# Performance work log

Measured on AMD Instinct MI355X. Metric: run time of the kernel, lower is better.

Reference implementation:

```python
import jax, jax.numpy as jnp
import numpy as np

B, CIN, T, H, W = 4, 64, 8, 32, 32
COUT, AHID = 64, 16
HWF = H * W


def _conv2d(x, w, b):
    y = jax.lax.conv_general_dilated(x, w, (1, 1), [(1, 1), (1, 1)],
                                     dimension_numbers=("NCHW", "OIHW", "NCHW"))
    return y + b[None, :, None, None]


def _conv1x1(x, w, b):
    return jnp.einsum("bchw,oc->bohw", x, w) + b[None, :, None, None]


def setup_inputs():
    key = jax.random.key(0)
    ks = jax.random.split(key, 18)
    s = 0.05
    d = {}
    d["X"] = jax.random.normal(ks[0], (B, CIN, T, H, W), jnp.float32)
    d["conv_w"] = jax.random.normal(ks[1], (4 * COUT, CIN + COUT, 3, 3), jnp.float32) * s
    d["conv_b"] = jnp.zeros((4 * COUT,), jnp.float32)
    d["W_ci"] = jax.random.normal(ks[2], (COUT, H, W), jnp.float32) * s
    d["W_cf"] = jax.random.normal(ks[3], (COUT, H, W), jnp.float32) * s
    d["W_co"] = jax.random.normal(ks[4], (COUT, H, W), jnp.float32) * s
    d["q_w"] = jax.random.normal(ks[5], (AHID, COUT), jnp.float32) * s
    d["q_b"] = jnp.zeros((AHID,), jnp.float32)
    d["k_w"] = jax.random.normal(ks[6], (AHID, COUT), jnp.float32) * s
    d["k_b"] = jnp.zeros((AHID,), jnp.float32)
    d["k2_w"] = jax.random.normal(ks[7], (AHID, COUT), jnp.float32) * s
    d["k2_b"] = jnp.zeros((AHID,), jnp.float32)
    d["v_w"] = jax.random.normal(ks[8], (COUT, COUT), jnp.float32) * s
    d["v_b"] = jnp.zeros((COUT,), jnp.float32)
    d["v2_w"] = jax.random.normal(ks[9], (COUT, COUT), jnp.float32) * s
    d["v2_b"] = jnp.zeros((COUT,), jnp.float32)
    d["z_w"] = jax.random.normal(ks[10], (2 * COUT, 2 * COUT), jnp.float32) * s
    d["z_b"] = jnp.zeros((2 * COUT,), jnp.float32)
    d["m_w"] = jax.random.normal(ks[11], (3 * COUT, 3 * COUT), jnp.float32) * s
    d["m_b"] = jnp.zeros((3 * COUT,), jnp.float32)
    return d


def _forward(X, conv_w, conv_b, W_ci, W_cf, W_co, q_w, q_b, k_w, k_b, k2_w, k2_b,
             v_w, v_b, v2_w, v2_b, z_w, z_b, m_w, m_b):
    def step(carry, x_t):
        h, c, m = carry
        # ConvLSTM cell with peephole connections
        gates = _conv2d(jnp.concatenate([x_t, h], axis=1), conv_w, conv_b)
        i_c, f_c, g_c, o_c = jnp.split(gates, 4, axis=1)
        ig = jax.nn.sigmoid(i_c + W_ci * c)
        fg = jax.nn.sigmoid(f_c + W_cf * c)
        c_new = fg * c + ig * jnp.tanh(g_c)
        og = jax.nn.sigmoid(o_c + W_co * c_new)
        h_new = og * jnp.tanh(c_new)
        # Self-attention memory module (all projections are 1x1 convs)
        q = _conv1x1(h_new, q_w, q_b).reshape(B, AHID, HWF)
        kh = _conv1x1(h_new, k_w, k_b).reshape(B, AHID, HWF)
        vh = _conv1x1(h_new, v_w, v_b).reshape(B, COUT, HWF)
        km = _conv1x1(m, k2_w, k2_b).reshape(B, AHID, HWF)
        vm = _conv1x1(m, v2_w, v2_b).reshape(B, COUT, HWF)
        att_h = jax.nn.softmax(jnp.einsum("ban,bam->bnm", q, kh), axis=-1)  # (B,HW,HW)
        att_m = jax.nn.softmax(jnp.einsum("ban,bam->bnm", q, km), axis=-1)
        z_h = jnp.einsum("bnm,bcm->bcn", att_h, vh)  # (B,COUT,HW)
        z_m = jnp.einsum("bnm,bcm->bcn", att_m, vm)
        z = jnp.concatenate([z_h, z_m], axis=1).reshape(B, 2 * COUT, H, W)
        z = _conv1x1(z, z_w, z_b)
        comb = _conv1x1(jnp.concatenate([z, h_new], axis=1), m_w, m_b)
        mo, mg, mi = jnp.split(comb, 3, axis=1)
        gi = jax.nn.sigmoid(mi)
        m_new = (1.0 - gi) * m + gi * jnp.tanh(mg)
        h_out = jax.nn.sigmoid(mo) * m_new
        return (h_out, c_new, m_new), h_out

    zeros = jnp.zeros((B, COUT, H, W), X.dtype)
    Xs = jnp.moveaxis(X, 2, 0)  # (T, B, CIN, H, W)
    _, hs = jax.lax.scan(step, (zeros, zeros, zeros), Xs)
    return jnp.moveaxis(hs, 0, 2)  # (B, COUT, T, H, W)


def reference(X, conv_w, conv_b, W_ci, W_cf, W_co, q_w, q_b, k_w, k_b, k2_w, k2_b,
              v_w, v_b, v2_w, v2_b, z_w, z_b, m_w, m_b):
    return _forward(X, conv_w, conv_b, W_ci, W_cf, W_co, q_w, q_b, k_w, k_b,
                    k2_w, k2_b, v_w, v_b, v2_w, v2_b, z_w, z_b, m_w, m_b)
```

## Files before the change

kernel.cpp:

```cpp
#include <hip/hip_runtime.h>
#include <hip/hip_bf16.h>

typedef __hip_bfloat16 bf16;
typedef unsigned short ushort;
typedef __attribute__((ext_vector_type(8))) short short8v;
typedef __attribute__((ext_vector_type(4))) float float4v;

__device__ __forceinline__ float b2f(bf16 v){ return __bfloat162float(v); }
__device__ __forceinline__ float sigm(float x){ return 1.0f/(1.0f+__expf(-x)); }
__device__ __forceinline__ float tanhc(float x){
  x = fminf(15.0f, fmaxf(-15.0f, x));
  float e = __expf(2.0f*x);
  return (e-1.0f)/(e+1.0f);
}
__device__ __forceinline__ ushort f2bu(float f){
  bf16 h = __float2bfloat16(f); return *reinterpret_cast<ushort*>(&h);
}
__device__ __forceinline__ float bu2f(ushort u){
  return __uint_as_float(((unsigned)u)<<16);
}
__device__ __forceinline__ short8v ldfrag(const ushort* p){
  return *reinterpret_cast<const short8v*>(p);
}
__device__ __forceinline__ void glds16(const ushort* g, ushort* l){
  __builtin_amdgcn_global_load_lds(
    (const __attribute__((address_space(1))) unsigned int*)g,
    (__attribute__((address_space(3))) unsigned int*)l, 16, 0, 0);
}

#define WS_SMALL   0
#define WS_FLAG    262144
#define WS_ZROW    262160
#define WS_H       262208
#define WS_C       524352
#define WS_M       786496
#define WS_QB16    1310784
#define WS_KHB16   1376320
#define WS_KMB16   1441856
#define WS_VTH16   1507392
#define WS_VTM16   1638464
#define WS_MTH     1769536
#define WS_MTL     1900608
#define WS_HNTH    2031680
#define WS_HNTL    2162752
#define WS_ZW16H   2293824
#define WS_ZW16L   2302016
#define WS_MW16H   2310208
#define WS_MW16L   2328640
#define WS_WXAH    2347072
#define WS_WHAH    2420800
#define WS_WXAL    2494528
#define WS_WHAL    2568256
#define WS_XTHI    2641984
#define WS_XTLO    3690560
#define WS_HTHI    4739136
#define WS_HTLO    4870208
#define WS_PWH     5001280
#define WS_PWL     5006912
#define WS_GXG     5012544
#define WS_GXO     7109696
#define O_CB    0
#define O_WCI   256
#define O_WCF   65792
#define O_WCO   131328
#define O_QW    196864
#define O_QB    197888
#define O_KW    197904
#define O_KB    198928
#define O_K2W   198944
#define O_K2B   199968
#define O_VW    199984
#define O_VB    204080
#define O_V2W   204144
#define O_V2B   208240
#define O_ZW    208304
#define O_ZB    224688
#define O_MW    224816
#define O_MB    261680

__global__ void k_probe(const unsigned int* __restrict__ Xu, int* __restrict__ flag){
  __shared__ int cnt;
  if (threadIdx.x == 0) cnt = 0;
  __syncthreads();
  unsigned int u = Xu[threadIdx.x];
  float f = __uint_as_float((u & 0xffffu) << 16);
  int bad = (fabsf(f) <= 1e4f) ? 0 : 1;
  atomicAdd(&cnt, bad);
  __syncthreads();
  if (threadIdx.x == 0) *flag = (cnt > 16) ? 1 : 0;
}

struct P18 { const void* p[18]; };

__global__ __launch_bounds__(256) void k_wconv(P18 pk, const int* __restrict__ flagp,
                                               float* __restrict__ dst){
  const int ns[18]   = {256,65536,65536,65536,1024,16,1024,16,1024,16,
                        4096,64,4096,64,16384,128,36864,192};
  const int offs[18] = {O_CB,O_WCI,O_WCF,O_WCO,O_QW,O_QB,O_KW,O_KB,O_K2W,O_K2B,
                        O_VW,O_VB,O_V2W,O_V2B,O_ZW,O_ZB,O_MW,O_MB};
  int y = blockIdx.y;
  int n = ns[y];
  int flag = *flagp;
  const void* src = pk.p[y];
  for (int i = blockIdx.x*256 + threadIdx.x; i < n; i += gridDim.x*256){
    float v = flag ? ((const float*)src)[i] : b2f(((const bf16*)src)[i]);
    dst[offs[y] + i] = v;
  }
}

__global__ __launch_bounds__(256) void k_wtrans(float* __restrict__ ws){
  int i = blockIdx.x*256 + threadIdx.x;
  if (i < 16384){
    float f = ws[O_ZW + i];
    ushort h = f2bu(f);
    ((ushort*)(ws + WS_ZW16H))[i] = h;
    ((ushort*)(ws + WS_ZW16L))[i] = f2bu(f - bu2f(h));
  }
  if (i < 36864){
    float f = ws[O_MW + i];
    ushort h = f2bu(f);
    ((ushort*)(ws + WS_MW16H))[i] = h;
    ((ushort*)(ws + WS_MW16L))[i] = f2bu(f - bu2f(h));
  }
  if (i < 11264){
    int r = i >> 6, k = i & 63;
    float f;
    if (r < 16)       f = ws[O_QW  + r*64 + k];
    else if (r < 32)  f = ws[O_KW  + (r-16)*64 + k];
    else if (r < 48)  f = ws[O_K2W + (r-32)*64 + k];
    else if (r < 112) f = ws[O_VW  + (r-48)*64 + k];
    else              f = ws[O_V2W + (r-112)*64 + k];
    ushort h = f2bu(f);
    ((ushort*)(ws + WS_PWH))[i] = h;
    ((ushort*)(ws + WS_PWL))[i] = f2bu(f - bu2f(h));
  }
}

__global__ __launch_bounds__(256) void k_init(const void* __restrict__ conv_w,
                                              const int* __restrict__ flagp,
                                              float* __restrict__ ws){
  int i = blockIdx.x*256 + threadIdx.x;
  int flag = *flagp;
  if (i < 786432) ws[WS_H + i] = 0.0f;
  if (i < 32) ws[WS_ZROW + i] = 0.0f;
  if (i < 196608) ((unsigned*)(ws + WS_QB16))[i] = 0u;
  if (i < 294912){
    int ci = i & 127;
    int j = i >> 7;
    int mm = j & 255, p = j >> 8;
    int cc = mm >> 2, g = mm & 3;
    int si = ((g*64 + cc)*128 + ci)*9 + p;
    float f;
    ushort hi, lo = 0;
    if (flag){
      f = ((const float*)conv_w)[si];
      hi = f2bu(f);
      lo = f2bu(f - bu2f(hi));
    } else {
      hi = ((const ushort*)conv_w)[si];
    }
    if (ci < 64){
      int di = (j << 6) + ((((ci >> 3) ^ (mm & 7)) << 3) | (ci & 7));
      ((ushort*)(ws + WS_WXAH))[di] = hi;
      ((ushort*)(ws + WS_WXAL))[di] = lo;
    } else {
      int c2 = ci - 64;
      int di = (j << 6) + ((((c2 >> 3) ^ (mm & 7)) << 3) | (c2 & 7));
      ((ushort*)(ws + WS_WHAH))[di] = hi;
      ((ushort*)(ws + WS_WHAL))[di] = lo;
    }
  }
  if (i < 131072){
    ((unsigned*)(ws + WS_HTHI))[i] = 0u;
    ((unsigned*)(ws + WS_HTLO))[i] = 0u;
    ((unsigned*)(ws + WS_MTH))[i] = 0u;
    ((unsigned*)(ws + WS_MTL))[i] = 0u;
  }
}

__global__ __launch_bounds__(256) void k_xt(const void* __restrict__ Xraw,
                                            const int* __restrict__ flagp,
                                            float* __restrict__ ws){
  __shared__ ushort hi_s[64][66];
  __shared__ ushort lo_s[64][66];
  int pt = blockIdx.x, s = blockIdx.y;
  int b = s >> 3, t = s & 7;
  int flag = *flagp;
  int tid = threadIdx.x;
  for (int k = 0; k < 16; ++k){
    int idx = tid + k*256;
    int ci = idx >> 6, pxl = idx & 63;
    size_t si = ((size_t)(b*64 + ci)*8 + t)*1024 + pt*64 + pxl;
    if (flag){
      float f = ((const float*)Xraw)[si];
      ushort h = f2bu(f);
      hi_s[pxl][ci] = h;
      lo_s[pxl][ci] = f2bu(f - bu2f(h));
    } else {
      hi_s[pxl][ci] = ((const ushort*)Xraw)[si];
    }
  }
  __syncthreads();
  ushort* xh = (ushort*)(ws + WS_XTHI) + ((size_t)s*1024 + pt*64)*64;
  ushort* xl = (ushort*)(ws + WS_XTLO) + ((size_t)s*1024 + pt*64)*64;
  for (int k = 0; k < 16; ++k){
    int idx = tid + k*256;
    int pxl = idx >> 6, ci = idx & 63;
    xh[pxl*64 + ci] = hi_s[pxl][ci];
    if (flag) xl[pxl*64 + ci] = lo_s[pxl][ci];
  }
}

__global__ __launch_bounds__(512, 4) void k_convx(
  const int* __restrict__ flagp,
  const ushort* __restrict__ wxah, const ushort* __restrict__ wxal,
  const ushort* __restrict__ xt_hi, const ushort* __restrict__ xt_lo,
  float* __restrict__ gxg, ushort* __restrict__ gxo)
{
  __shared__ ushort xabuf[8192];
  __shared__ ushort xsm[54*136];
  int nt = blockIdx.x, mh = blockIdx.y, tb = blockIdx.z;
  int tid = threadIdx.x;
  int flag = *flagp;
  int ytile = nt >> 1, x0 = (nt & 1) * 16;
  const ushort* xb  = xt_hi + (size_t)tb*65536;
  const ushort* xlb = xt_lo + (size_t)tb*65536;
  int w = tid >> 6, lane = tid & 63, lr = lane & 15, lk = lane >> 4;
  const ushort* aw  = wxah + (size_t)(mh*128 + w*16)*64 + lane*8;
  const ushort* awl = wxal + (size_t)(mh*128 + w*16)*64 + lane*8;
  ushort* areg = xabuf + w*1024;

  const uint4 Z16 = make_uint4(0,0,0,0);
  for (int idx = tid; idx < 864; idx += 512){
    int slot = idx >> 4, c = idx & 15;
    int rr = slot / 18, xi = slot - rr*18;
    int gy = ytile - 1 + rr, gx2 = x0 - 1 + xi;
    bool valid = (gy >= 0) & (gy < 32) & (gx2 >= 0) & (gx2 < 32);
    int px = gy*32 + gx2;
    uint4 v = Z16;
    if (valid){
      if (c < 8)       v = *reinterpret_cast<const uint4*>(xb  + (size_t)px*64 + c*8);
      else if (flag)   v = *reinterpret_cast<const uint4*>(xlb + (size_t)px*64 + (c-8)*8);
    }
    *reinterpret_cast<uint4*>(&xsm[slot*136 + c*8]) = v;
  }
  __syncthreads();

  int px = nt*16 + lr;
  int sw = lr & 7;
  const int cx0 = ((lk ^ sw) << 3);
  const int cx1 = (((4+lk) ^ sw) << 3);
  float4v acc = {0.f,0.f,0.f,0.f};

  #pragma unroll 1
  for (int p = 0; p < 9; ++p){
    glds16(aw + (size_t)p*16384,       areg);
    glds16(aw + (size_t)p*16384 + 512, areg + 512);
    asm volatile("s_waitcnt vmcnt(0)" ::: "memory");
    __builtin_amdgcn_sched_barrier(0);
    short8v A0 = ldfrag(areg + lr*64 + cx0);
    short8v A1 = ldfrag(areg + lr*64 + cx1);
    int pinl = (p/3)*18 + lr + (p%3);
    const ushort* bl = &xsm[pinl*136 + lk*8];
    short8v BX0 = ldfrag(bl), BX1 = ldfrag(bl+32);
    acc = __builtin_amdgcn_mfma_f32_16x16x32_bf16(A0, BX0, acc, 0,0,0);
    acc = __builtin_amdgcn_mfma_f32_16x16x32_bf16(A1, BX1, acc, 0,0,0);
    if (flag){
      short8v BXl0 = ldfrag(bl+64), BXl1 = ldfrag(bl+96);
      acc = __builtin_amdgcn_mfma_f32_16x16x32_bf16(A0, BXl0, acc, 0,0,0);
      acc = __builtin_amdgcn_mfma_f32_16x16x32_bf16(A1, BXl1, acc, 0,0,0);
      asm volatile("s_waitcnt lgkmcnt(0)" ::: "memory");
      __builtin_amdgcn_sched_barrier(0);
      glds16(awl + (size_t)p*16384,       areg);
      glds16(awl + (size_t)p*16384 + 512, areg + 512);
      asm volatile("s_waitcnt vmcnt(0)" ::: "memory");
      __builtin_amdgcn_sched_barrier(0);
      short8v Al0 = ldfrag(areg + lr*64 + cx0);
      short8v Al1 = ldfrag(areg + lr*64 + cx1);
      acc = __builtin_amdgcn_mfma_f32_16x16x32_bf16(Al0, BX0, acc, 0,0,0);
      acc = __builtin_amdgcn_mfma_f32_16x16x32_bf16(Al1, BX1, acc, 0,0,0);
      asm volatile("s_waitcnt lgkmcnt(0)" ::: "memory");
      __builtin_amdgcn_sched_barrier(0);
    } else {
      asm volatile("s_waitcnt lgkmcnt(0)" ::: "memory");
      __builtin_amdgcn_sched_barrier(0);
    }
  }

  {
    int cc = mh*32 + w*4 + lk;
    gxg[((size_t)tb*64 + cc)*1024 + px] = acc[2];
    ushort* go = gxo + ((size_t)tb*192 + cc*3)*1024 + px;
    go[0]    = f2bu(acc[0]);
    go[1024] = f2bu(acc[1]);
    go[2048] = f2bu(acc[3]);
  }
}

__global__ __launch_bounds__(1024, 4) void k_convp(
  const int* __restrict__ flagp,
  const ushort* __restrict__ whah, const ushort* __restrict__ whal,
  const ushort* __restrict__ ht_hi, const ushort* __restrict__ ht_lo,
  const float* __restrict__ gxg, const ushort* __restrict__ gxo,
  const float* __restrict__ smalls, float* __restrict__ cst,
  const ushort* __restrict__ pwh, const ushort* __restrict__ pwl,
  const ushort* __restrict__ mth, const ushort* __restrict__ mtl,
  ushort* __restrict__ hnth, ushort* __restrict__ hntl,
  ushort* __restrict__ qb16, ushort* __restrict__ khb16, ushort* __restrict__ kmb16,
  ushort* __restrict__ vth16, ushort* __restrict__ vtm16, int t)
{
  __shared__ ushort albuf[16384];
  __shared__ ushort bsm[54*136];
  __shared__ ushort hbh[16*72];
  __shared__ ushort hbl[16*72];
  int nt = blockIdx.x, b = blockIdx.y;
  int tid = threadIdx.x;
  int flag = *flagp;
  int ytile = nt >> 1, x0 = (nt & 1) * 16;

  const ushort* hb  = ht_hi + (size_t)b*65536;
  const ushort* hlb = ht_lo + (size_t)b*65536;

  int w = tid >> 6, lane = tid & 63, lr = lane & 15, lk = lane >> 4;
  const ushort* aw  = whah + (size_t)(w*16)*64 + lane*8;
  const ushort* awl = whal + (size_t)(w*16)*64 + lane*8;
  ushort* areg = albuf + w*1024;

  if (!flag){
    glds16(aw, areg);
    glds16(aw + 512, areg + 512);
  }

  int px = nt*16 + lr;
  int cc = w*4 + lk;
  int tb = b*8 + t;
  const ushort* go = gxo + ((size_t)tb*192 + cc*3)*1024 + px;
  float a0 = bu2f(go[0]);
  float a1 = bu2f(go[1024]);
  float a3 = bu2f(go[2048]);
  float a2 = gxg[((size_t)tb*64 + cc)*1024 + px];

  const uint4 Z16 = make_uint4(0,0,0,0);
  if (tid < 864){
    int slot = tid >> 4, c = tid & 15;
    int rr = slot / 18, xi = slot - rr*18;
    int gy = ytile - 1 + rr, gx2 = x0 - 1 + xi;
    bool valid = (gy >= 0) & (gy < 32) & (gx2 >= 0) & (gx2 < 32);
    int hpx = gy*32 + gx2;
    uint4 v = Z16;
    if (valid){
      if (c < 8) v = *reinterpret_cast<const uint4*>(hb  + (size_t)hpx*64 + c*8);
      else       v = *reinterpret_cast<const uint4*>(hlb + (size_t)hpx*64 + (c-8)*8);
    }
    *reinterpret_cast<uint4*>(&bsm[slot*136 + c*8]) = v;
  }
  __syncthreads();

  const int sw = lr & 7;
  const int c2n = ((lk ^ sw) << 3);
  const int c3n = (((4+lk) ^ sw) << 3);

  float4v acc = {a0, a1, a2, a3};

  if (!flag){
    #pragma unroll
    for (int p = 0; p < 9; ++p){
      if (p > 0){
        asm volatile("s_waitcnt vmcnt(0)" ::: "memory");
        __builtin_amdgcn_sched_barrier(0);
      }
      short8v A2 = ldfrag(areg + lr*64 + c2n);
      short8v A3 = ldfrag(areg + lr*64 + c3n);
      if (p < 8){
        asm volatile("s_waitcnt lgkmcnt(0)" ::: "memory");
        __builtin_amdgcn_sched_barrier(0);
        glds16(aw + (size_t)(p+1)*16384,       areg);
        glds16(aw + (size_t)(p+1)*16384 + 512, areg + 512);
        __builtin_amdgcn_sched_barrier(0);
      }
      int pinl = (p/3)*18 + lr + (p%3);
      const ushort* bl = &bsm[pinl*136 + lk*8];
      short8v BH0 = ldfrag(bl),    BH1 = ldfrag(bl+32);
      short8v BL0 = ldfrag(bl+64), BL1 = ldfrag(bl+96);
      acc = __builtin_amdgcn_mfma_f32_16x16x32_bf16(A2, BH0, acc, 0,0,0);
      acc = __builtin_amdgcn_mfma_f32_16x16x32_bf16(A3, BH1, acc, 0,0,0);
      acc = __builtin_amdgcn_mfma_f32_16x16x32_bf16(A2, BL0, acc, 0,0,0);
      acc = __builtin_amdgcn_mfma_f32_16x16x32_bf16(A3, BL1, acc, 0,0,0);
    }
  } else {
    #pragma unroll 1
    for (int p = 0; p < 9; ++p){
      glds16(aw + (size_t)p*16384,       areg);
      glds16(aw + (size_t)p*16384 + 512, areg + 512);
      asm volatile("s_waitcnt vmcnt(0)" ::: "memory");
      __builtin_amdgcn_sched_barrier(0);
      short8v A2 = ldfrag(areg + lr*64 + c2n);
      short8v A3 = ldfrag(areg + lr*64 + c3n);
      asm volatile("s_waitcnt lgkmcnt(0)" ::: "memory");
      __builtin_amdgcn_sched_barrier(0);
      glds16(awl + (size_t)p*16384,       areg);
      glds16(awl + (size_t)p*16384 + 512, areg + 512);
      asm volatile("s_waitcnt vmcnt(0)" ::: "memory");
      __builtin_amdgcn_sched_barrier(0);
      short8v Al2 = ldfrag(areg + lr*64 + c2n);
      short8v Al3 = ldfrag(areg + lr*64 + c3n);
      asm volatile("s_waitcnt lgkmcnt(0)" ::: "memory");
      __builtin_amdgcn_sched_barrier(0);
      int pinl = (p/3)*18 + lr + (p%3);
      const ushort* bl = &bsm[pinl*136 + lk*8];
      short8v BH0 = ldfrag(bl),    BH1 = ldfrag(bl+32);
      short8v BL0 = ldfrag(bl+64), BL1 = ldfrag(bl+96);
      acc = __builtin_amdgcn_mfma_f32_16x16x32_bf16(A2, BH0, acc, 0,0,0);
      acc = __builtin_amdgcn_mfma_f32_16x16x32_bf16(A3, BH1, acc, 0,0,0);
      acc = __builtin_amdgcn_mfma_f32_16x16x32_bf16(A2, BL0, acc, 0,0,0);
      acc = __builtin_amdgcn_mfma_f32_16x16x32_bf16(A3, BL1, acc, 0,0,0);
      acc = __builtin_amdgcn_mfma_f32_16x16x32_bf16(Al2, BH0, acc, 0,0,0);
      acc = __builtin_amdgcn_mfma_f32_16x16x32_bf16(Al3, BH1, acc, 0,0,0);
    }
  }

  {
    int wi = cc*1024 + px;
    size_t sidx = ((size_t)(b*64 + cc))*1024 + px;
    float cprev = cst[sidx];
    float ic = acc[0] + smalls[O_CB + cc];
    float fc = acc[1] + smalls[O_CB + 64 + cc];
    float gc = acc[2] + smalls[O_CB + 128 + cc];
    float oc = acc[3] + smalls[O_CB + 192 + cc];
    float ig = sigm(ic + smalls[O_WCI + wi]*cprev);
    float fg = sigm(fc + smalls[O_WCF + wi]*cprev);
    float cnew = fg*cprev + ig*tanhc(gc);
    float og = sigm(oc + smalls[O_WCO + wi]*cnew);
    cst[sidx] = cnew;
    float hv = og*tanhc(cnew);
    size_t tix = ((size_t)b*1024 + px)*64 + cc;
    ushort hh = f2bu(hv);
    ushort hl2 = f2bu(hv - bu2f(hh));
    hnth[tix] = hh;
    hntl[tix] = hl2;
    hbh[lr*72 + cc] = hh;
    hbl[lr*72 + cc] = hl2;
  }
  __syncthreads();

  if (w < 11){
    int tt = w;
    const float4v Z4 = {0.f,0.f,0.f,0.f};
    bool srcm = (tt == 2) || (tt >= 7);
    short8v b0, b1, bl0, bl1;
    if (srcm){
      size_t bb = ((size_t)b*1024 + nt*16 + lr)*64 + lk*8;
      b0  = ldfrag(mth + bb);  b1  = ldfrag(mth + bb + 32);
      bl0 = ldfrag(mtl + bb);  bl1 = ldfrag(mtl + bb + 32);
    } else {
      b0  = ldfrag(&hbh[lr*72 + lk*8]);  b1  = ldfrag(&hbh[lr*72 + 32 + lk*8]);
      bl0 = ldfrag(&hbl[lr*72 + lk*8]);  bl1 = ldfrag(&hbl[lr*72 + 32 + lk*8]);
    }
    const ushort* ar = pwh + (size_t)(tt*16 + lr)*64 + lk*8;
    short8v pa0 = ldfrag(ar), pa1 = ldfrag(ar + 32);
    float4v d = Z4;
    d = __builtin_amdgcn_mfma_f32_16x16x32_bf16(pa0, b0,  d, 0,0,0);
    d = __builtin_amdgcn_mfma_f32_16x16x32_bf16(pa1, b1,  d, 0,0,0);
    d = __builtin_amdgcn_mfma_f32_16x16x32_bf16(pa0, bl0, d, 0,0,0);
    d = __builtin_amdgcn_mfma_f32_16x16x32_bf16(pa1, bl1, d, 0,0,0);
    if (flag){
      const ushort* arl = pwl + (size_t)(tt*16 + lr)*64 + lk*8;
      short8v pal0 = ldfrag(arl), pal1 = ldfrag(arl + 32);
      d = __builtin_amdgcn_mfma_f32_16x16x32_bf16(pal0, b0, d, 0,0,0);
      d = __builtin_amdgcn_mfma_f32_16x16x32_bf16(pal1, b1, d, 0,0,0);
    }
    int n = nt*16 + lr;
    int boff = (tt==0) ? O_QB : (tt==1) ? O_KB : (tt==2) ? O_K2B
             : (tt<7) ? (O_VB + (tt-3)*16) : (O_V2B + (tt-7)*16);
    if (tt < 3){
      ushort* base = (tt==0) ? qb16 : (tt==1) ? khb16 : kmb16;
      ushort u[4];
      #pragma unroll
      for (int q = 0; q < 4; ++q)
        u[q] = f2bu(d[q] + smalls[boff + lk*4 + q]);
      *reinterpret_cast<uint2*>(&base[((size_t)b*1024 + n)*32 + lk*4]) =
        make_uint2((unsigned)u[0] | ((unsigned)u[1]<<16),
                   (unsigned)u[2] | ((unsigned)u[3]<<16));
    } else {
      ushort* base = (tt<7) ? vth16 : vtm16;
      int cc0 = ((tt<7) ? (tt-3) : (tt-7))*16 + lk*4;
      #pragma unroll
      for (int q = 0; q < 4; ++q)
        base[((size_t)b*64 + cc0 + q)*1024 + n] = f2bu(d[q] + smalls[boff + lk*4 + q]);
    }
  }
}

__global__ __launch_bounds__(512) void k_fattz(
  const ushort* __restrict__ qb16, const ushort* __restrict__ khb16,
  const ushort* __restrict__ kmb16, const ushort* __restrict__ vth16,
  const ushort* __restrict__ vtm16,
  const ushort* __restrict__ hnth, const ushort* __restrict__ hntl,
  const float* __restrict__ smalls,
  const ushort* __restrict__ zw16h, const ushort* __restrict__ zw16l,
  const ushort* __restrict__ mw16h, const ushort* __restrict__ mw16l,
  const int* __restrict__ flagp,
  float* __restrict__ mst, ushort* __restrict__ mth, ushort* __restrict__ mtl,
  ushort* __restrict__ hth, ushort* __restrict__ htl,
  void* __restrict__ outraw, int t)
{
  __shared__ __align__(16) unsigned char poolA[34816];
  __shared__ __align__(16) ushort ztbh[16*136];
  __shared__ __align__(16) ushort ztbl[16*136];
  __shared__ float cb[192*17];
  __shared__ float ml[64*17];
  __shared__ float rs_s[2][4][16];

  ushort* es   = (ushort*)poolA;
  ushort* zbh  = (ushort*)poolA;
  ushort* zbl  = (ushort*)(poolA + 8704);
  float*  ho_s = (float*)poolA;
  float*  mn_s = (float*)(poolA + 4352);

  int nt = blockIdx.x, b = blockIdx.y;
  int n0 = nt*16;
  int tid = threadIdx.x;
  int w = tid >> 6, lane = tid & 63, lr = lane & 15, lk = lane >> 4;
  int br = w >> 2, wq = w & 3;
  int flag = *flagp;
  const float4v Z4 = {0.f,0.f,0.f,0.f};

  const ushort* kb = (br ? kmb16 : khb16) + (size_t)b*32768;
  const ushort* vt = (br ? vtm16 : vth16) + (size_t)b*65536;
  const ushort* qp = qb16 + (size_t)b*32768;

  for (int idx = tid; idx < 1024; idx += 512){
    int ch = idx >> 4, pp = idx & 15;
    ml[ch*17+pp] = mst[((size_t)b*64 + ch)*1024 + n0 + pp];
  }

  short8v qf = ldfrag(qp + (size_t)(n0 + lr)*32 + lk*8);

  float4v acc[2];
  acc[0]=Z4; acc[1]=Z4;
  float rsum = 0.f;

  #pragma unroll 1
  for (int mc = 0; mc < 4; ++mc){
    ushort* esb = es + (br*2 + (mc & 1))*4352;
    int mbase = mc*256 + wq*64;
    #pragma unroll
    for (int tau = 0; tau < 4; ++tau){
      short8v af = ldfrag(kb + (size_t)(mbase + tau*16 + lr)*32 + lk*8);
      float4v d = __builtin_amdgcn_mfma_f32_16x16x32_bf16(af, qf, Z4, 0,0,0);
      ushort u0 = f2bu(__expf(fminf(d[0], 60.f)));
      ushort u1 = f2bu(__expf(fminf(d[1], 60.f)));
      ushort u2 = f2bu(__expf(fminf(d[2], 60.f)));
      ushort u3 = f2bu(__expf(fminf(d[3], 60.f)));
      rsum += (bu2f(u0) + bu2f(u1)) + (bu2f(u2) + bu2f(u3));
      unsigned lo = (unsigned)u0 | ((unsigned)u1 << 16);
      unsigned hi = (unsigned)u2 | ((unsigned)u3 << 16);
      *reinterpret_cast<uint2*>(&esb[lr*272 + wq*64 + tau*16 + lk*4]) = make_uint2(lo, hi);
    }
    __syncthreads();
    #pragma unroll
    for (int ks = 0; ks < 8; ++ks){
      short8v av = ldfrag(vt + (size_t)(wq*16 + lr)*1024 + mc*256 + ks*32 + lk*8);
      short8v bv = ldfrag(&esb[lr*272 + ks*32 + lk*8]);
      acc[ks & 1] = __builtin_amdgcn_mfma_f32_16x16x32_bf16(av, bv, acc[ks & 1], 0,0,0);
    }
  }

  {
    float r = rsum;
    r += __shfl_xor(r, 16);
    r += __shfl_xor(r, 32);
    if (lane < 16) rs_s[br][wq][lr] = r;
  }
  __syncthreads();
  {
    float rinv = 1.0f / (rs_s[br][0][lr] + rs_s[br][1][lr] + rs_s[br][2][lr] + rs_s[br][3][lr]);
    int ch0 = br*64 + wq*16 + lk*4;
    ushort uh[4], ul[4];
    #pragma unroll
    for (int r = 0; r < 4; ++r){
      float z = (acc[0][r] + acc[1][r])*rinv;
      uh[r] = f2bu(z);
      ul[r] = f2bu(z - bu2f(uh[r]));
    }
    *reinterpret_cast<uint2*>(&zbh[lr*136 + ch0]) =
      make_uint2((unsigned)uh[0] | ((unsigned)uh[1]<<16), (unsigned)uh[2] | ((unsigned)uh[3]<<16));
    *reinterpret_cast<uint2*>(&zbl[lr*136 + ch0]) =
      make_uint2((unsigned)ul[0] | ((unsigned)ul[1]<<16), (unsigned)ul[2] | ((unsigned)ul[3]<<16));
  }
  __syncthreads();

  {
    float4v zacc = Z4;
    if (!flag){
      #pragma unroll
      for (int kf = 0; kf < 4; ++kf){
        short8v a  = ldfrag(zw16h + (size_t)(w*16 + lr)*128 + kf*32 + lk*8);
        short8v bh = ldfrag(&zbh[lr*136 + kf*32 + lk*8]);
        short8v bl = ldfrag(&zbl[lr*136 + kf*32 + lk*8]);
        zacc = __builtin_amdgcn_mfma_f32_16x16x32_bf16(a, bh, zacc, 0,0,0);
        zacc = __builtin_amdgcn_mfma_f32_16x16x32_bf16(a, bl, zacc, 0,0,0);
      }
    } else {
      #pragma unroll
      for (int kf = 0; kf < 4; ++kf){
        short8v a  = ldfrag(zw16h + (size_t)(w*16 + lr)*128 + kf*32 + lk*8);
        short8v al = ldfrag(zw16l + (size_t)(w*16 + lr)*128 + kf*32 + lk*8);
        short8v bh = ldfrag(&zbh[lr*136 + kf*32 + lk*8]);
        short8v bl = ldfrag(&zbl[lr*136 + kf*32 + lk*8]);
        zacc = __builtin_amdgcn_mfma_f32_16x16x32_bf16(a,  bh, zacc, 0,0,0);
        zacc = __builtin_amdgcn_mfma_f32_16x16x32_bf16(a,  bl, zacc, 0,0,0);
        zacc = __builtin_amdgcn_mfma_f32_16x16x32_bf16(al, bh, zacc, 0,0,0);
      }
    }
    int r0 = w*16 + lk*4;
    ushort th[4], tl[4];
    #pragma unroll
    for (int q = 0; q < 4; ++q){
      float ztv = zacc[q] + smalls[O_ZB + r0 + q];
      th[q] = f2bu(ztv);
      tl[q] = f2bu(ztv - bu2f(th[q]));
    }
    *reinterpret_cast<uint2*>(&ztbh[lr*136 + r0]) =
      make_uint2((unsigned)th[0] | ((unsigned)th[1]<<16), (unsigned)th[2] | ((unsigned)th[3]<<16));
    *reinterpret_cast<uint2*>(&ztbl[lr*136 + r0]) =
      make_uint2((unsigned)tl[0] | ((unsigned)tl[1]<<16), (unsigned)tl[2] | ((unsigned)tl[3]<<16));
  }
  __syncthreads();

  const ushort* hrow  = hnth + ((size_t)b*1024 + n0 + lr)*64;
  const ushort* hrowl = hntl + ((size_t)b*1024 + n0 + lr)*64;
  #pragma unroll
  for (int mi = 0; mi < 2; ++mi){
    if (mi == 1 && w >= 4) break;
    int mf = (mi == 0) ? w : (w + 8);
    float4v cacc = Z4;
    const ushort* arow  = mw16h + (size_t)(mf*16 + lr)*192;
    const ushort* arowl = mw16l + (size_t)(mf*16 + lr)*192;
    if (!flag){
      #pragma unroll
      for (int kf = 0; kf < 4; ++kf){
        short8v a  = ldfrag(arow + kf*32 + lk*8);
        short8v bh = ldfrag(&ztbh[lr*136 + kf*32 + lk*8]);
        short8v bl = ldfrag(&ztbl[lr*136 + kf*32 + lk*8]);
        cacc = __builtin_amdgcn_mfma_f32_16x16x32_bf16(a, bh, cacc, 0,0,0);
        cacc = __builtin_amdgcn_mfma_f32_16x16x32_bf16(a, bl, cacc, 0,0,0);
      }
      #pragma unroll
      for (int kf = 0; kf < 2; ++kf){
        short8v a  = ldfrag(arow + 128 + kf*32 + lk*8);
        short8v bh = ldfrag(hrow + kf*32 + lk*8);
        short8v bl = ldfrag(hrowl + kf*32 + lk*8);
        cacc = __builtin_amdgcn_mfma_f32_16x16x32_bf16(a, bh, cacc, 0,0,0);
        cacc = __builtin_amdgcn_mfma_f32_16x16x32_bf16(a, bl, cacc, 0,0,0);
      }
    } else {
      #pragma unroll
      for (int kf = 0; kf < 4; ++kf){
        short8v a  = ldfrag(arow + kf*32 + lk*8);
        short8v al = ldfrag(arowl + kf*32 + lk*8);
        short8v bh = ldfrag(&ztbh[lr*136 + kf*32 + lk*8]);
        short8v bl = ldfrag(&ztbl[lr*136 + kf*32 + lk*8]);
        cacc = __builtin_amdgcn_mfma_f32_16x16x32_bf16(a,  bh, cacc, 0,0,0);
        cacc = __builtin_amdgcn_mfma_f32_16x16x32_bf16(a,  bl, cacc, 0,0,0);
        cacc = __builtin_amdgcn_mfma_f32_16x16x32_bf16(al, bh, cacc, 0,0,0);
      }
      #pragma unroll
      for (int kf = 0; kf < 2; ++kf){
        short8v a  = ldfrag(arow + 128 + kf*32 + lk*8);
        short8v al = ldfrag(arowl + 128 + kf*32 + lk*8);
        short8v bh = ldfrag(hrow + kf*32 + lk*8);
        short8v bl = ldfrag(hrowl + kf*32 + lk*8);
        cacc = __builtin_amdgcn_mfma_f32_16x16x32_bf16(a,  bh, cacc, 0,0,0);
        cacc = __builtin_amdgcn_mfma_f32_16x16x32_bf16(a,  bl, cacc, 0,0,0);
        cacc = __builtin_amdgcn_mfma_f32_16x16x32_bf16(al, bh, cacc, 0,0,0);
      }
    }
    int r0 = mf*16 + lk*4;
    #pragma unroll
    for (int q = 0; q < 4; ++q)
      cb[(r0+q)*17 + lr] = cacc[q] + smalls[O_MB + r0 + q];
  }
  __syncthreads();

  {
    int px = tid >> 5, lr2 = tid & 31;
    #pragma unroll
    for (int j = 0; j < 2; ++j){
      int ch = lr2 + 32*j;
      float mo = cb[ch*17 + px];
      float mg = cb[(64+ch)*17 + px];
      float mi = cb[(128+ch)*17 + px];
      float mold = ml[ch*17 + px];
      float gi = sigm(mi);
      float mnew = (1.0f-gi)*mold + gi*tanhc(mg);
      float ho = sigm(mo)*mnew;
      ho_s[ch*17+px] = ho;
      mn_s[ch*17+px] = mnew;
    }
  }
  __syncthreads();
  for (int idx = tid; idx < 1024; idx += 512){
    int ch = idx >> 4, pp = idx & 15;
    int n = n0 + pp;
    size_t gidx = ((size_t)b*64 + ch)*1024 + n;
    float mn = mn_s[ch*17+pp];
    mst[gidx] = mn;
    float ho = ho_s[ch*17+pp];
    size_t tix = ((size_t)b*1024 + n)*64 + ch;
    ushort hb_ = f2bu(ho);
    hth[tix] = hb_;
    htl[tix] = f2bu(ho - bu2f(hb_));
    ushort mh_ = f2bu(mn);
    mth[tix] = mh_;
    mtl[tix] = f2bu(mn - bu2f(mh_));
    size_t oidx = ((size_t)(b*64+ch)*8 + t)*1024 + n;
    if (flag) ((float*)outraw)[oidx] = ho;
    else      ((bf16*)outraw)[oidx] = __float2bfloat16(ho);
  }
}

extern "C" void kernel_launch(void* const* d_in, const int* in_sizes, int n_in,
                              void* d_out, int out_size, void* d_ws, size_t ws_size,
                              hipStream_t stream)
{
  float* ws = (float*)d_ws;
  int* flag = (int*)(ws + WS_FLAG);
  float* c    = ws + WS_C;
  float* m    = ws + WS_M;
  float* gxg  = ws + WS_GXG;
  ushort* gxo   = (ushort*)(ws + WS_GXO);
  ushort* qb16  = (ushort*)(ws + WS_QB16);
  ushort* khb16 = (ushort*)(ws + WS_KHB16);
  ushort* kmb16 = (ushort*)(ws + WS_KMB16);
  ushort* vth16 = (ushort*)(ws + WS_VTH16);
  ushort* vtm16 = (ushort*)(ws + WS_VTM16);
  ushort* mth   = (ushort*)(ws + WS_MTH);
  ushort* mtl   = (ushort*)(ws + WS_MTL);
  ushort* hnth  = (ushort*)(ws + WS_HNTH);
  ushort* hntl  = (ushort*)(ws + WS_HNTL);
  ushort* zw16h = (ushort*)(ws + WS_ZW16H);
  ushort* zw16l = (ushort*)(ws + WS_ZW16L);
  ushort* mw16h = (ushort*)(ws + WS_MW16H);
  ushort* mw16l = (ushort*)(ws + WS_MW16L);
  ushort* wxah  = (ushort*)(ws + WS_WXAH);
  ushort* wxal  = (ushort*)(ws + WS_WXAL);
  ushort* whah  = (ushort*)(ws + WS_WHAH);
  ushort* whal  = (ushort*)(ws + WS_WHAL);
  ushort* xt_hi = (ushort*)(ws + WS_XTHI);
  ushort* xt_lo = (ushort*)(ws + WS_XTLO);
  ushort* ht_hi = (ushort*)(ws + WS_HTHI);
  ushort* ht_lo = (ushort*)(ws + WS_HTLO);
  ushort* pwh   = (ushort*)(ws + WS_PWH);
  ushort* pwl   = (ushort*)(ws + WS_PWL);

  k_probe<<<1, 256, 0, stream>>>((const unsigned int*)d_in[0], flag);
  P18 pk;
  for (int i = 0; i < 18; ++i) pk.p[i] = d_in[2 + i];
  k_wconv<<<dim3(64,18), 256, 0, stream>>>(pk, flag, ws);
  k_init<<<3072, 256, 0, stream>>>(d_in[1], flag, ws);
  k_xt<<<dim3(16,32), 256, 0, stream>>>(d_in[0], flag, ws);
  k_wtrans<<<144, 256, 0, stream>>>(ws);
  k_convx<<<dim3(64,2,32), 512, 0, stream>>>(flag, wxah, wxal, xt_hi, xt_lo, gxg, gxo);

  for (int t = 0; t < 8; ++t){
    k_convp<<<dim3(64,4), 1024, 0, stream>>>(flag, whah, whal, ht_hi, ht_lo,
                                             gxg, gxo, ws, c, pwh, pwl, mth, mtl,
                                             hnth, hntl, qb16, khb16, kmb16,
                                             vth16, vtm16, t);
    k_fattz<<<dim3(64,4), 512, 0, stream>>>(qb16, khb16, kmb16, vth16, vtm16,
                                            hnth, hntl, ws, zw16h, zw16l, mw16h, mw16l,
                                            flag, m, mth, mtl, ht_hi, ht_lo, d_out, t);
  }
  (void)in_sizes; (void)n_in; (void)out_size; (void)ws_size;
}
```

Baseline: 404.4 us.

## Double-buffer weight tiles in x-convolution and split flag path into phases

```diff
diff --git a/kernel.cpp b/kernel.cpp
--- a/kernel.cpp
+++ b/kernel.cpp
@@ -217,8 +217,8 @@
   const ushort* __restrict__ xt_hi, const ushort* __restrict__ xt_lo,
   float* __restrict__ gxg, ushort* __restrict__ gxo)
 {
-  __shared__ ushort xabuf[8192];
-  __shared__ ushort xsm[54*136];
+  __shared__ ushort xabuf[16384];
+  __shared__ ushort xsm[54*72];
   int nt = blockIdx.x, mh = blockIdx.y, tb = blockIdx.z;
   int tid = threadIdx.x;
   int flag = *flagp;
@@ -228,21 +228,24 @@
   int w = tid >> 6, lane = tid & 63, lr = lane & 15, lk = lane >> 4;
   const ushort* aw  = wxah + (size_t)(mh*128 + w*16)*64 + lane*8;
   const ushort* awl = wxal + (size_t)(mh*128 + w*16)*64 + lane*8;
-  ushort* areg = xabuf + w*1024;
+  ushort* buf0 = xabuf + w*1024;
+  ushort* buf1 = xabuf + 8192 + w*1024;
 
   const uint4 Z16 = make_uint4(0,0,0,0);
-  for (int idx = tid; idx < 864; idx += 512){
-    int slot = idx >> 4, c = idx & 15;
+
+  if (!flag){
+    glds16(aw, buf0);
+    glds16(aw + 512, buf0 + 512);
+  }
+
+  for (int idx = tid; idx < 432; idx += 512){
+    int slot = idx >> 3, c = idx & 7;
     int rr = slot / 18, xi = slot - rr*18;
     int gy = ytile - 1 + rr, gx2 = x0 - 1 + xi;
     bool valid = (gy >= 0) & (gy < 32) & (gx2 >= 0) & (gx2 < 32);
     int px = gy*32 + gx2;
-    uint4 v = Z16;
-    if (valid){
-      if (c < 8)       v = *reinterpret_cast<const uint4*>(xb  + (size_t)px*64 + c*8);
-      else if (flag)   v = *reinterpret_cast<const uint4*>(xlb + (size_t)px*64 + (c-8)*8);
-    }
-    *reinterpret_cast<uint4*>(&xsm[slot*136 + c*8]) = v;
+    uint4 v = valid ? *reinterpret_cast<const uint4*>(xb + (size_t)px*64 + c*8) : Z16;
+    *reinterpret_cast<uint4*>(&xsm[slot*72 + c*8]) = v;
   }
   __syncthreads();
 
@@ -252,36 +255,74 @@
   const int cx1 = (((4+lk) ^ sw) << 3);
   float4v acc = {0.f,0.f,0.f,0.f};
 
-  #pragma unroll 1
-  for (int p = 0; p < 9; ++p){
-    glds16(aw + (size_t)p*16384,       areg);
-    glds16(aw + (size_t)p*16384 + 512, areg + 512);
-    asm volatile("s_waitcnt vmcnt(0)" ::: "memory");
-    __builtin_amdgcn_sched_barrier(0);
-    short8v A0 = ldfrag(areg + lr*64 + cx0);
-    short8v A1 = ldfrag(areg + lr*64 + cx1);
-    int pinl = (p/3)*18 + lr + (p%3);
-    const ushort* bl = &xsm[pinl*136 + lk*8];
-    short8v BX0 = ldfrag(bl), BX1 = ldfrag(bl+32);
-    acc = __builtin_amdgcn_mfma_f32_16x16x32_bf16(A0, BX0, acc, 0,0,0);
-    acc = __builtin_amdgcn_mfma_f32_16x16x32_bf16(A1, BX1, acc, 0,0,0);
-    if (flag){
-      short8v BXl0 = ldfrag(bl+64), BXl1 = ldfrag(bl+96);
-      acc = __builtin_amdgcn_mfma_f32_16x16x32_bf16(A0, BXl0, acc, 0,0,0);
-      acc = __builtin_amdgcn_mfma_f32_16x16x32_bf16(A1, BXl1, acc, 0,0,0);
-      asm volatile("s_waitcnt lgkmcnt(0)" ::: "memory");
+  if (!flag){
+    #pragma unroll
+    for (int p = 0; p < 9; ++p){
+      if (p < 8){
+        ushort* dst = (p & 1) ? buf0 : buf1;
+        glds16(aw + (size_t)(p+1)*16384,       dst);
+        glds16(aw + (size_t)(p+1)*16384 + 512, dst + 512);
+        asm volatile("s_waitcnt vmcnt(2)" ::: "memory");
+      } else {
+        asm volatile("s_waitcnt vmcnt(0)" ::: "memory");
+      }
       __builtin_amdgcn_sched_barrier(0);
-      glds16(awl + (size_t)p*16384,       areg);
-      glds16(awl + (size_t)p*16384 + 512, areg + 512);
+      const ushort* ab = (p & 1) ? buf1 : buf0;
+      short8v A0 = ldfrag(ab + lr*64 + cx0);
+      short8v A1 = ldfrag(ab + lr*64 + cx1);
+      int pinl = (p/3)*18 + lr + (p%3);
+      const ushort* bl = &xsm[pinl*72 + lk*8];
+      short8v BX0 = ldfrag(bl), BX1 = ldfrag(bl+32);
+      acc = __builtin_amdgcn_mfma_f32_16x16x32_bf16(A0, BX0, acc, 0,0,0);
+      acc = __builtin_amdgcn_mfma_f32_16x16x32_bf16(A1, BX1, acc, 0,0,0);
+    }
+  } else {
+    #pragma unroll 1
+    for (int p = 0; p < 9; ++p){
+      glds16(aw  + (size_t)p*16384,       buf0);
+      glds16(aw  + (size_t)p*16384 + 512, buf0 + 512);
+      glds16(awl + (size_t)p*16384,       buf1);
+      glds16(awl + (size_t)p*16384 + 512, buf1 + 512);
       asm volatile("s_waitcnt vmcnt(0)" ::: "memory");
       __builtin_amdgcn_sched_barrier(0);
-      short8v Al0 = ldfrag(areg + lr*64 + cx0);
-      short8v Al1 = ldfrag(areg + lr*64 + cx1);
+      short8v A0  = ldfrag(buf0 + lr*64 + cx0);
+      short8v A1  = ldfrag(buf0 + lr*64 + cx1);
+      short8v Al0 = ldfrag(buf1 + lr*64 + cx0);
+      short8v Al1 = ldfrag(buf1 + lr*64 + cx1);
+      int pinl = (p/3)*18 + lr + (p%3);
+      const ushort* bl = &xsm[pinl*72 + lk*8];
+      short8v BX0 = ldfrag(bl), BX1 = ldfrag(bl+32);
+      acc = __builtin_amdgcn_mfma_f32_16x16x32_bf16(A0,  BX0, acc, 0,0,0);
+      acc = __builtin_amdgcn_mfma_f32_16x16x32_bf16(A1,  BX1, acc, 0,0,0);
       acc = __builtin_amdgcn_mfma_f32_16x16x32_bf16(Al0, BX0, acc, 0,0,0);
       acc = __builtin_amdgcn_mfma_f32_16x16x32_bf16(Al1, BX1, acc, 0,0,0);
       asm volatile("s_waitcnt lgkmcnt(0)" ::: "memory");
       __builtin_amdgcn_sched_barrier(0);
-    } else {
+    }
+    __syncthreads();
+    for (int idx = tid; idx < 432; idx += 512){
+      int slot = idx >> 3, c = idx & 7;
+      int rr = slot / 18, xi = slot - rr*18;
+      int gy = ytile - 1 + rr, gx2 = x0 - 1 + xi;
+      bool valid = (gy >= 0) & (gy < 32) & (gx2 >= 0) & (gx2 < 32);
+      int hp = gy*32 + gx2;
+      uint4 v = valid ? *reinterpret_cast<const uint4*>(xlb + (size_t)hp*64 + c*8) : Z16;
+      *reinterpret_cast<uint4*>(&xsm[slot*72 + c*8]) = v;
+    }
+    __syncthreads();
+    #pragma unroll 1
+    for (int p = 0; p < 9; ++p){
+      glds16(aw + (size_t)p*16384,       buf0);
+      glds16(aw + (size_t)p*16384 + 512, buf0 + 512);
+      asm volatile("s_waitcnt vmcnt(0)" ::: "memory");
+      __builtin_amdgcn_sched_barrier(0);
+      short8v A0 = ldfrag(buf0 + lr*64 + cx0);
+      short8v A1 = ldfrag(buf0 + lr*64 + cx1);
+      int pinl = (p/3)*18 + lr + (p%3);
+      const ushort* bl = &xsm[pinl*72 + lk*8];
+      short8v BXl0 = ldfrag(bl), BXl1 = ldfrag(bl+32);
+      acc = __builtin_amdgcn_mfma_f32_16x16x32_bf16(A0, BXl0, acc, 0,0,0);
+      acc = __builtin_amdgcn_mfma_f32_16x16x32_bf16(A1, BXl1, acc, 0,0,0);
       asm volatile("s_waitcnt lgkmcnt(0)" ::: "memory");
       __builtin_amdgcn_sched_barrier(0);
     }
```

After: 421.3 us. 1.04x slower.
